# Kernel optimization log

Hardware: AMD Instinct MI355X
Metric: run time of the kernel (lower is better)

The kernel has to match this reference:

```python
import jax, jax.numpy as jnp
import numpy as np

B = 2            # batch_size (number of windows)
W_SIZE = 2       # window_size
WIDTH = 256      # cart_pixel_width
TEMP = 0.01      # softmax_temp
EPS = 1e-12      # F.normalize eps


def _l2norm(x, axis):
    n = jnp.sqrt(jnp.sum(x * x, axis=axis, keepdims=True))
    return x / jnp.maximum(n, EPS)


def _bilinear(img, u, v):
    """align_corners=True bilinear sample. img: [C,H,W]; u,v: [N] pixel coords."""
    H, W = img.shape[-2], img.shape[-1]
    u0 = jnp.clip(jnp.floor(u), 0, W - 1)
    v0 = jnp.clip(jnp.floor(v), 0, H - 1)
    u1 = jnp.clip(u0 + 1, 0, W - 1)
    v1 = jnp.clip(v0 + 1, 0, H - 1)
    au = u - u0
    av = v - v0
    u0i, u1i = u0.astype(jnp.int32), u1.astype(jnp.int32)
    v0i, v1i = v0.astype(jnp.int32), v1.astype(jnp.int32)
    g = lambda vi, ui: img[:, vi, ui]  # [C,N]
    return (g(v0i, u0i) * (1 - au) * (1 - av) + g(v0i, u1i) * au * (1 - av)
            + g(v1i, u0i) * (1 - au) * av + g(v1i, u1i) * au * av)


def setup_inputs() -> dict:
    key = jax.random.key(0)
    k1, k2, k3, k4 = jax.random.split(key, 4)
    BW, C, N, S = B * W_SIZE, 248, 1024, 1
    return {
        "keypoint_scores": jax.random.normal(k1, (BW, S, N), dtype=jnp.float32),
        "keypoint_desc": jax.random.normal(k2, (BW, C, N), dtype=jnp.float32),
        "desc_dense": jax.random.normal(k3, (BW, C, WIDTH, WIDTH), dtype=jnp.float32),
        "times_img": jax.random.uniform(k4, (BW, 1, WIDTH, WIDTH), dtype=jnp.float32),
    }


def reference(keypoint_scores, keypoint_desc, desc_dense, times_img):
    BW, C, N = keypoint_desc.shape
    w = W_SIZE
    # frame index bookkeeping (same as the torch per-batch loop, vectorized)
    src_ids = jnp.arange(B) * w                                   # [B]
    tgt_ids = (jnp.arange(B)[:, None] * w
               + jnp.arange(1, w)[None, :]).reshape(-1)           # [B*(w-1)]

    # dense pixel coordinates [W^2, 2] in (u, v) order
    v, u = jnp.meshgrid(jnp.arange(WIDTH), jnp.arange(WIDTH), indexing='ij')
    coords = jnp.stack([u.reshape(-1), v.reshape(-1)], axis=1).astype(desc_dense.dtype)

    # normalized source dense descriptors [B, C, W^2]
    src = _l2norm(desc_dense[src_ids].reshape(B, C, -1), axis=1)
    # normalized target keypoint descriptors [B, w-1, C, N]
    tgt = _l2norm(keypoint_desc[tgt_ids].reshape(B, w - 1, C, N), axis=2)

    # dense correlation: [B, w-1, N, W^2]
    match_vals = jnp.einsum('bkcn,bcm->bknm', tgt, src)
    soft = jax.nn.softmax(match_vals / TEMP, axis=-1)
    # coordinate-weighted sum -> pseudo coords [B*(w-1), N, 2]
    pseudo_coords = jnp.einsum('bknm,md->bknd', soft, coords).reshape(B * (w - 1), N, 2)

    # bilinear-sample src times at pseudo coords (normalize->grid_sample round trip
    # with align_corners maps back to the same pixel coords; H == W here)
    src_times = jnp.repeat(times_img[src_ids], w - 1, axis=0)      # [B*(w-1),1,H,W]
    pseudo_times = jax.vmap(_bilinear)(src_times,
                                       pseudo_coords[..., 0],
                                       pseudo_coords[..., 1])      # [B*(w-1),1,N]

    return (pseudo_coords, keypoint_scores[tgt_ids], tgt_ids, pseudo_times)
```

## Files before the change

kernel.cpp:

```cpp
#include <hip/hip_runtime.h>
#include <math.h>

typedef int i32x4 __attribute__((ext_vector_type(4)));
typedef int i32x16 __attribute__((ext_vector_type(16)));

#define CC 248
#define MM 65536
#define NN 1024

__device__ __forceinline__ float fexp2(float x) { return __builtin_amdgcn_exp2f(x); }


__global__ __launch_bounds__(512)
void convB_kernel(const float* __restrict__ dense, char* __restrict__ Ag) {
    __shared__ char at[2][16][128][16];
    __shared__ float scr[4][128];
    const int bid = blockIdx.x;
    const int fb  = bid >> 9;
    const int p0  = (bid & 511) * 128;
    const int tid = threadIdx.x;
    const int row = tid & 127;
    const int q   = tid >> 7;

    const float* dptr = dense + (size_t)(2 * fb) * CC * MM + p0 + row;
    float v[64];
    float ss = 0.f;
#pragma unroll
    for (int i = 0; i < 64; ++i) {
        int c = q * 64 + i;
        float x = (c < CC) ? dptr[(size_t)c * MM] : 0.f;
        v[i] = x;
        ss += x * x;
    }
    scr[q][row] = ss;
    __syncthreads();
    float inv = 32768.0f / fmaxf(sqrtf(scr[0][row] + scr[1][row] + scr[2][row] + scr[3][row]), 1e-12f);

#pragma unroll
    for (int j = 0; j < 16; ++j) {
        unsigned w1 = 0, w0 = 0;
#pragma unroll
        for (int t = 0; t < 4; ++t) {
            float qv = fminf(fmaxf(rintf(v[j * 4 + t] * inv), -32768.f), 32639.f);
            int af = (int)qv;
            int a1 = (af + 128) >> 8;
            int a0 = af - (a1 << 8);
            w1 |= (unsigned)(a1 & 255) << (8 * t);
            w0 |= (unsigned)(a0 & 255) << (8 * t);
        }
        int c0 = q * 64 + j * 4;
        int kg = c0 >> 4, dw = (c0 >> 2) & 3;
        *(unsigned*)&at[0][kg][row][dw * 4] = w1;
        *(unsigned*)&at[1][kg][row][dw * 4] = w0;
    }
    __syncthreads();

    const int tile = p0 >> 8, rhalf = (p0 >> 7) & 1;
    char* outb = Ag + (size_t)(fb * 256 + tile) * 131072;
#pragma unroll
    for (int it = 0; it < 8; ++it) {
        int id = tid + it * 512;
        int pl = id >> 11, kg = (id >> 7) & 15, r2 = id & 127;
        i32x4 vv = *(const i32x4*)&at[pl][kg][r2][0];
        *(i32x4*)&outb[(size_t)pl * 65536 + kg * 4096 + (rhalf * 128 + r2) * 16] = vv;
    }
}

__global__ __launch_bounds__(256)
void convA_kernel(const float* __restrict__ kdesc, char* __restrict__ Bg) {
    __shared__ char bt[2][16][32][16];
    __shared__ float scr[8][32];
    const int bid = blockIdx.x;
    const int b   = bid >> 5;
    const int nt  = bid & 31;
    const int n0  = nt * 32;
    const int tid = threadIdx.x;
    const int col = tid & 31;
    const int q   = tid >> 5;

    const float* kp = kdesc + (size_t)(2 * b + 1) * CC * NN + n0 + col;
    float ss = 0.f;
    for (int i = 0; i < 31; ++i) {
        int c = q * 31 + i;
        float v = kp[(size_t)c * NN];
        ss += v * v;
    }
    scr[q][col] = ss;
    __syncthreads();
    float tot = 0.f;
#pragma unroll
    for (int k = 0; k < 8; ++k) tot += scr[k][col];
    float inv = 32768.0f / fmaxf(sqrtf(tot), 1e-12f);
    if (tid < 64) {
        int pl = tid >> 5, c2 = tid & 31;
        *(long*)&bt[pl][15][c2][8] = 0L;
    }
    __syncthreads();
    for (int i = 0; i < 31; ++i) {
        int c = q * 31 + i;
        float qq = fminf(fmaxf(rintf(kp[(size_t)c * NN] * inv), -32768.f), 32639.f);
        int af = (int)qq;
        int a1 = (af + 128) >> 8;
        int a0 = af - (a1 << 8);
        bt[0][c >> 4][col][c & 15] = (char)a1;
        bt[1][c >> 4][col][c & 15] = (char)a0;
    }
    __syncthreads();
    char* outb = Bg + (size_t)(b * 32 + nt) * 16384;
    const char* src = &bt[0][0][0][0];
#pragma unroll
    for (int it = 0; it < 4; ++it) {
        int id = tid + it * 256;
        *(i32x4*)&outb[(size_t)id * 16] = *(const i32x4*)&src[(size_t)id * 16];
    }
}

__global__ __launch_bounds__(256, 2)
void gemm_kernel(const char* __restrict__ Ag, const char* __restrict__ Bg,
                 float* __restrict__ partials) {
    __shared__ char lds[24576];

    const int bid  = blockIdx.x;
    const int xcd  = bid & 7;
    const int rest = bid >> 3;
    const int nchunk = rest & 3;
    const int pid  = xcd + 8 * (rest >> 2);
    const int b      = pid >> 6;
    const int mchunk = pid & 63;

    const int lane = threadIdx.x & 63;
    const int w    = threadIdx.x >> 6;
    const int lrow = lane & 31;
    const int lhi  = lane >> 5;

    const char* atile0 = Ag + ((size_t)b * 256 + mchunk * 4) * 131072;
    const char* bb     = Bg + (size_t)(b * 32 + nchunk * 8 + w * 2) * 16384;

    i32x4 bc[8][2][2];
#pragma unroll
    for (int kk = 0; kk < 8; ++kk)
#pragma unroll
        for (int pl = 0; pl < 2; ++pl)
#pragma unroll
            for (int bp = 0; bp < 2; ++bp)
                bc[kk][pl][bp] = *(const i32x4*)(bb + bp * 16384 + pl * 8192
                                                 + (kk * 2 + lhi) * 512 + lrow * 16);

    auto ISSUE = [&](int p, int slotOff) {
        const int mtn = p >> 1, h = p & 1;
        const int tile = mtn >> 3, row0 = (mtn & 7) * 32;
#pragma unroll
        for (int i = 0; i < 2; ++i) {
            int c = w * 2 + i;
            int pl = c >> 2, kkl = c & 3;
            const char* src = atile0 + (size_t)tile * 131072 + pl * 65536
                            + (h * 8 + kkl * 2 + lhi) * 4096 + (row0 + lrow) * 16;
            char* dst = &lds[slotOff + pl * 4096 + kkl * 1024];
            __builtin_amdgcn_global_load_lds(
                (const __attribute__((address_space(1))) void*)src,
                (__attribute__((address_space(3))) void*)dst, 16, 0, 0);
        }
    };

    i32x16 accH[2], accX[2];
#pragma unroll
    for (int bp = 0; bp < 2; ++bp) { accH[bp] = (i32x16)(0); accX[bp] = (i32x16)(0); }
    float rz[2] = {0.f, 0.f}, rsu[2] = {0.f, 0.f}, rsv[2] = {0.f, 0.f};

    const float S2 = 100.0f * 1.4426950408889634f / 1073741824.0f;
    const float cH = 65536.0f * S2;
    const float cX = 256.0f * S2;
    const float BASE = 145.0f;

    auto EPI = [&](int mtq) {
        const int mbase = mchunk * 1024 + mtq * 32;
        const float ub = (float)((mbase & 255) + 4 * lhi);
        const float vcoord = (float)(mbase >> 8);
#pragma unroll
        for (int bp = 0; bp < 2; ++bp) {
            float tz = 0.f, tsur = 0.f;
#pragma unroll
            for (int r = 0; r < 16; ++r) {
                float e = fexp2(fmaf((float)accH[bp][r], cH,
                                fmaf((float)accX[bp][r], cX, -BASE)));
                tz += e;
                tsur = fmaf(e, (float)((r & 3) + 8 * (r >> 2)), tsur);
            }
            rz[bp] += tz;
            rsu[bp] += fmaf(ub, tz, tsur);
            rsv[bp] = fmaf(vcoord, tz, rsv[bp]);
            accH[bp] = (i32x16)(0); accX[bp] = (i32x16)(0);
        }
    };

    ISSUE(0, 0);
    ISSUE(1, 8192);
    int slotR = 0, slotW = 16384;

    for (int mt = 0; mt < 32; ++mt) {
#pragma unroll
        for (int h = 0; h < 2; ++h) {
            const int p = mt * 2 + h;
            if (p < 63) asm volatile("s_waitcnt vmcnt(2)" ::: "memory");
            else        asm volatile("s_waitcnt vmcnt(0)" ::: "memory");
            asm volatile("s_barrier" ::: "memory");
            if (p + 2 < 64) ISSUE(p + 2, slotW);

            i32x4 a1_0 = *(const i32x4*)&lds[slotR + 0 * 1024 + lhi * 512 + lrow * 16];
            i32x4 a0_0 = *(const i32x4*)&lds[slotR + 4096 + 0 * 1024 + lhi * 512 + lrow * 16];
            i32x4 a1_1 = *(const i32x4*)&lds[slotR + 1 * 1024 + lhi * 512 + lrow * 16];
            i32x4 a0_1 = *(const i32x4*)&lds[slotR + 4096 + 1 * 1024 + lhi * 512 + lrow * 16];

            if (h == 0 && mt > 0) EPI(mt - 1);

            __builtin_amdgcn_s_setprio(1);
#pragma unroll
            for (int bp = 0; bp < 2; ++bp) {
                accH[bp] = __builtin_amdgcn_mfma_i32_32x32x32_i8(a1_0, bc[h * 4 + 0][0][bp], accH[bp], 0, 0, 0);
                accX[bp] = __builtin_amdgcn_mfma_i32_32x32x32_i8(a1_0, bc[h * 4 + 0][1][bp], accX[bp], 0, 0, 0);
                accX[bp] = __builtin_amdgcn_mfma_i32_32x32x32_i8(a0_0, bc[h * 4 + 0][0][bp], accX[bp], 0, 0, 0);
                accH[bp] = __builtin_amdgcn_mfma_i32_32x32x32_i8(a1_1, bc[h * 4 + 1][0][bp], accH[bp], 0, 0, 0);
                accX[bp] = __builtin_amdgcn_mfma_i32_32x32x32_i8(a1_1, bc[h * 4 + 1][1][bp], accX[bp], 0, 0, 0);
                accX[bp] = __builtin_amdgcn_mfma_i32_32x32x32_i8(a0_1, bc[h * 4 + 1][0][bp], accX[bp], 0, 0, 0);
            }
            __builtin_amdgcn_s_setprio(0);

            i32x4 a1_2 = *(const i32x4*)&lds[slotR + 2 * 1024 + lhi * 512 + lrow * 16];
            i32x4 a0_2 = *(const i32x4*)&lds[slotR + 4096 + 2 * 1024 + lhi * 512 + lrow * 16];
            i32x4 a1_3 = *(const i32x4*)&lds[slotR + 3 * 1024 + lhi * 512 + lrow * 16];
            i32x4 a0_3 = *(const i32x4*)&lds[slotR + 4096 + 3 * 1024 + lhi * 512 + lrow * 16];

            __builtin_amdgcn_s_setprio(1);
#pragma unroll
            for (int bp = 0; bp < 2; ++bp) {
                accH[bp] = __builtin_amdgcn_mfma_i32_32x32x32_i8(a1_2, bc[h * 4 + 2][0][bp], accH[bp], 0, 0, 0);
                accX[bp] = __builtin_amdgcn_mfma_i32_32x32x32_i8(a1_2, bc[h * 4 + 2][1][bp], accX[bp], 0, 0, 0);
                accX[bp] = __builtin_amdgcn_mfma_i32_32x32x32_i8(a0_2, bc[h * 4 + 2][0][bp], accX[bp], 0, 0, 0);
                accH[bp] = __builtin_amdgcn_mfma_i32_32x32x32_i8(a1_3, bc[h * 4 + 3][0][bp], accH[bp], 0, 0, 0);
                accX[bp] = __builtin_amdgcn_mfma_i32_32x32x32_i8(a1_3, bc[h * 4 + 3][1][bp], accX[bp], 0, 0, 0);
                accX[bp] = __builtin_amdgcn_mfma_i32_32x32x32_i8(a0_3, bc[h * 4 + 3][0][bp], accX[bp], 0, 0, 0);
            }
            __builtin_amdgcn_s_setprio(0);

            slotR = (slotR == 16384) ? 0 : slotR + 8192;
            slotW = (slotW == 16384) ? 0 : slotW + 8192;
        }
    }
    EPI(31);

#pragma unroll
    for (int bp = 0; bp < 2; ++bp) {
        rz[bp]  += __shfl_xor(rz[bp],  32, 64);
        rsu[bp] += __shfl_xor(rsu[bp], 32, 64);
        rsv[bp] += __shfl_xor(rsv[bp], 32, 64);
    }
    if (lane < 32) {
#pragma unroll
        for (int bp = 0; bp < 2; ++bp) {
            int n = nchunk * 256 + w * 64 + bp * 32 + lrow;
            size_t idxp = ((size_t)b * NN + n) * 64 + mchunk;
            ((float4*)partials)[idxp] = make_float4(rz[bp], rsu[bp], rsv[bp], 0.f);
        }
    }
}

__global__ __launch_bounds__(256)
void combine_kernel(const float* __restrict__ partials,
                    const float* __restrict__ kscores,
                    const float* __restrict__ times,
                    float* __restrict__ out) {
    const int wg   = blockIdx.x * 4 + (threadIdx.x >> 6);
    const int lane = threadIdx.x & 63;
    const int b = wg >> 10, n = wg & 1023;
    const float4* pp = (const float4*)partials + (size_t)wg * 64;

    float4 p = pp[lane];
    float z = p.x, su = p.y, sv = p.z;
#pragma unroll
    for (int mask = 32; mask >= 1; mask >>= 1) {
        z  += __shfl_xor(z,  mask, 64);
        su += __shfl_xor(su, mask, 64);
        sv += __shfl_xor(sv, mask, 64);
    }

    if (lane == 0) {
        float u = su / z, v = sv / z;
        out[(size_t)wg * 2 + 0] = u;
        out[(size_t)wg * 2 + 1] = v;
        out[4096 + wg] = kscores[(size_t)(2 * b + 1) * NN + n];
        if (wg == 0) { out[6144] = 1.0f; out[6145] = 3.0f; }

        const float* timg = times + (size_t)(2 * b) * MM;
        float u0 = fminf(fmaxf(floorf(u), 0.f), 255.f);
        float v0 = fminf(fmaxf(floorf(v), 0.f), 255.f);
        float u1 = fminf(u0 + 1.f, 255.f);
        float v1 = fminf(v0 + 1.f, 255.f);
        float au = u - u0, av = v - v0;
        int u0i = (int)u0, u1i = (int)u1, v0i = (int)v0, v1i = (int)v1;
        float t00 = timg[v0i * 256 + u0i], t01 = timg[v0i * 256 + u1i];
        float t10 = timg[v1i * 256 + u0i], t11 = timg[v1i * 256 + u1i];
        float t = t00 * (1.f - au) * (1.f - av) + t01 * au * (1.f - av)
                + t10 * (1.f - au) * av + t11 * au * av;
        out[6146 + wg] = t;
    }
}

extern "C" void kernel_launch(void* const* d_in, const int* in_sizes, int n_in,
                              void* d_out, int out_size, void* d_ws, size_t ws_size,
                              hipStream_t stream) {
    const float* kscores = (const float*)d_in[0];
    const float* kdesc   = (const float*)d_in[1];
    const float* dense   = (const float*)d_in[2];
    const float* times   = (const float*)d_in[3];
    float* out = (float*)d_out;

    char* Ag = (char*)d_ws;
    char* Bg = Ag + (size_t)2 * 256 * 131072;
    float* partials = (float*)(Bg + (size_t)2 * 32 * 16384);

    hipLaunchKernelGGL(convB_kernel,   dim3(1024), dim3(512), 0, stream, dense, Ag);
    hipLaunchKernelGGL(convA_kernel,   dim3(64),   dim3(256), 0, stream, kdesc, Bg);
    hipLaunchKernelGGL(gemm_kernel,    dim3(512),  dim3(256), 0, stream, Ag, Bg, partials);
    hipLaunchKernelGGL(combine_kernel, dim3(512),  dim3(256), 0, stream, partials, kscores, times, out);
}
```

Baseline: 136.7 us.

## Fuse dense descriptor quantization into GEMM kernel, dropping global int8 intermediate

```diff
diff --git a/kernel.cpp b/kernel.cpp
--- a/kernel.cpp
+++ b/kernel.cpp
@@ -10,61 +10,6 @@
 
 __device__ __forceinline__ float fexp2(float x) { return __builtin_amdgcn_exp2f(x); }
 
-
-__global__ __launch_bounds__(512)
-void convB_kernel(const float* __restrict__ dense, char* __restrict__ Ag) {
-    __shared__ char at[2][16][128][16];
-    __shared__ float scr[4][128];
-    const int bid = blockIdx.x;
-    const int fb  = bid >> 9;
-    const int p0  = (bid & 511) * 128;
-    const int tid = threadIdx.x;
-    const int row = tid & 127;
-    const int q   = tid >> 7;
-
-    const float* dptr = dense + (size_t)(2 * fb) * CC * MM + p0 + row;
-    float v[64];
-    float ss = 0.f;
-#pragma unroll
-    for (int i = 0; i < 64; ++i) {
-        int c = q * 64 + i;
-        float x = (c < CC) ? dptr[(size_t)c * MM] : 0.f;
-        v[i] = x;
-        ss += x * x;
-    }
-    scr[q][row] = ss;
-    __syncthreads();
-    float inv = 32768.0f / fmaxf(sqrtf(scr[0][row] + scr[1][row] + scr[2][row] + scr[3][row]), 1e-12f);
-
-#pragma unroll
-    for (int j = 0; j < 16; ++j) {
-        unsigned w1 = 0, w0 = 0;
-#pragma unroll
-        for (int t = 0; t < 4; ++t) {
-            float qv = fminf(fmaxf(rintf(v[j * 4 + t] * inv), -32768.f), 32639.f);
-            int af = (int)qv;
-            int a1 = (af + 128) >> 8;
-            int a0 = af - (a1 << 8);
-            w1 |= (unsigned)(a1 & 255) << (8 * t);
-            w0 |= (unsigned)(a0 & 255) << (8 * t);
-        }
-        int c0 = q * 64 + j * 4;
-        int kg = c0 >> 4, dw = (c0 >> 2) & 3;
-        *(unsigned*)&at[0][kg][row][dw * 4] = w1;
-        *(unsigned*)&at[1][kg][row][dw * 4] = w0;
-    }
-    __syncthreads();
-
-    const int tile = p0 >> 8, rhalf = (p0 >> 7) & 1;
-    char* outb = Ag + (size_t)(fb * 256 + tile) * 131072;
-#pragma unroll
-    for (int it = 0; it < 8; ++it) {
-        int id = tid + it * 512;
-        int pl = id >> 11, kg = (id >> 7) & 15, r2 = id & 127;
-        i32x4 vv = *(const i32x4*)&at[pl][kg][r2][0];
-        *(i32x4*)&outb[(size_t)pl * 65536 + kg * 4096 + (rhalf * 128 + r2) * 16] = vv;
-    }
-}
 
 __global__ __launch_bounds__(256)
 void convA_kernel(const float* __restrict__ kdesc, char* __restrict__ Bg) {
@@ -116,150 +61,129 @@
 }
 
 __global__ __launch_bounds__(256, 2)
-void gemm_kernel(const char* __restrict__ Ag, const char* __restrict__ Bg,
-                 float* __restrict__ partials) {
-    __shared__ char lds[24576];
-
-    const int bid  = blockIdx.x;
-    const int xcd  = bid & 7;
-    const int rest = bid >> 3;
-    const int nchunk = rest & 3;
-    const int pid  = xcd + 8 * (rest >> 2);
-    const int b      = pid >> 6;
-    const int mchunk = pid & 63;
-
-    const int lane = threadIdx.x & 63;
-    const int w    = threadIdx.x >> 6;
+void fused_kernel(const float* __restrict__ dense, const char* __restrict__ Bg,
+                  float* __restrict__ partials) {
+    extern __shared__ char lds[];
+    float* scr = (float*)(lds + 65536);
+
+    const int bid = blockIdx.x;
+    const int fb  = bid >> 9;
+    const int p0  = (bid & 511) * 128;
+    const int tid = threadIdx.x;
+
+    {
+        const int row = tid & 127;
+        const int q   = tid >> 7;
+        const float* dptr = dense + (size_t)(2 * fb) * CC * MM + (size_t)(q * 124) * MM + p0 + row;
+        float v[124];
+        float ss = 0.f;
+#pragma unroll
+        for (int i = 0; i < 124; ++i) {
+            v[i] = dptr[(size_t)i * MM];
+            ss += v[i] * v[i];
+        }
+        scr[q * 128 + row] = ss;
+        *(long*)&lds[(tid >> 7) * 32768 + 15 * 2048 + (tid & 127) * 16 + 8] = 0L;
+        __syncthreads();
+        float inv = 32768.0f / fmaxf(sqrtf(scr[row] + scr[128 + row]), 1e-12f);
+#pragma unroll
+        for (int j = 0; j < 31; ++j) {
+            unsigned w1 = 0, w0 = 0;
+#pragma unroll
+            for (int t = 0; t < 4; ++t) {
+                float qv = fminf(fmaxf(rintf(v[j * 4 + t] * inv), -32768.f), 32639.f);
+                int af = (int)qv;
+                int a1 = (af + 128) >> 8;
+                int a0 = af - (a1 << 8);
+                w1 |= (unsigned)(a1 & 255) << (8 * t);
+                w0 |= (unsigned)(a0 & 255) << (8 * t);
+            }
+            int c0 = q * 124 + j * 4;
+            int kg = c0 >> 4, dw = (c0 >> 2) & 3;
+            *(unsigned*)&lds[kg * 2048 + row * 16 + dw * 4] = w1;
+            *(unsigned*)&lds[32768 + kg * 2048 + row * 16 + dw * 4] = w0;
+        }
+    }
+    __syncthreads();
+
+    const int lane = tid & 63;
+    const int w    = tid >> 6;
     const int lrow = lane & 31;
     const int lhi  = lane >> 5;
 
-    const char* atile0 = Ag + ((size_t)b * 256 + mchunk * 4) * 131072;
-    const char* bb     = Bg + (size_t)(b * 32 + nchunk * 8 + w * 2) * 16384;
-
-    i32x4 bc[8][2][2];
-#pragma unroll
-    for (int kk = 0; kk < 8; ++kk)
-#pragma unroll
-        for (int pl = 0; pl < 2; ++pl)
-#pragma unroll
-            for (int bp = 0; bp < 2; ++bp)
-                bc[kk][pl][bp] = *(const i32x4*)(bb + bp * 16384 + pl * 8192
-                                                 + (kk * 2 + lhi) * 512 + lrow * 16);
-
-    auto ISSUE = [&](int p, int slotOff) {
-        const int mtn = p >> 1, h = p & 1;
-        const int tile = mtn >> 3, row0 = (mtn & 7) * 32;
-#pragma unroll
-        for (int i = 0; i < 2; ++i) {
-            int c = w * 2 + i;
-            int pl = c >> 2, kkl = c & 3;
-            const char* src = atile0 + (size_t)tile * 131072 + pl * 65536
-                            + (h * 8 + kkl * 2 + lhi) * 4096 + (row0 + lrow) * 16;
-            char* dst = &lds[slotOff + pl * 4096 + kkl * 1024];
-            __builtin_amdgcn_global_load_lds(
-                (const __attribute__((address_space(1))) void*)src,
-                (__attribute__((address_space(3))) void*)dst, 16, 0, 0);
-        }
-    };
-
-    i32x16 accH[2], accX[2];
-#pragma unroll
-    for (int bp = 0; bp < 2; ++bp) { accH[bp] = (i32x16)(0); accX[bp] = (i32x16)(0); }
-    float rz[2] = {0.f, 0.f}, rsu[2] = {0.f, 0.f}, rsv[2] = {0.f, 0.f};
+    const char* bbase = Bg + (size_t)(fb * 32) * 16384;
 
     const float S2 = 100.0f * 1.4426950408889634f / 1073741824.0f;
     const float cH = 65536.0f * S2;
     const float cX = 256.0f * S2;
     const float BASE = 145.0f;
 
-    auto EPI = [&](int mtq) {
-        const int mbase = mchunk * 1024 + mtq * 32;
-        const float ub = (float)((mbase & 255) + 4 * lhi);
-        const float vcoord = (float)(mbase >> 8);
+    for (int nc = 0; nc < 4; ++nc) {
+        i32x4 bc[8][2][2];
+#pragma unroll
+        for (int kk = 0; kk < 8; ++kk)
+#pragma unroll
+            for (int pl = 0; pl < 2; ++pl)
+#pragma unroll
+                for (int bp = 0; bp < 2; ++bp)
+                    bc[kk][pl][bp] = *(const i32x4*)(bbase
+                        + (size_t)(w * 8 + nc * 2 + bp) * 16384 + pl * 8192
+                        + (kk * 2 + lhi) * 512 + lrow * 16);
+
+        float rz[2] = {0.f, 0.f}, rsu[2] = {0.f, 0.f}, rsv[2] = {0.f, 0.f};
+
+#pragma unroll
+        for (int mt = 0; mt < 4; ++mt) {
+            i32x16 accH[2], accX[2];
+#pragma unroll
+            for (int bp = 0; bp < 2; ++bp) { accH[bp] = (i32x16)(0); accX[bp] = (i32x16)(0); }
+
+#pragma unroll
+            for (int kk = 0; kk < 8; ++kk) {
+                i32x4 a1 = *(const i32x4*)&lds[(kk * 2 + lhi) * 2048 + (mt * 32 + lrow) * 16];
+                i32x4 a0 = *(const i32x4*)&lds[32768 + (kk * 2 + lhi) * 2048 + (mt * 32 + lrow) * 16];
+                __builtin_amdgcn_s_setprio(1);
+#pragma unroll
+                for (int bp = 0; bp < 2; ++bp) {
+                    accH[bp] = __builtin_amdgcn_mfma_i32_32x32x32_i8(a1, bc[kk][0][bp], accH[bp], 0, 0, 0);
+                    accX[bp] = __builtin_amdgcn_mfma_i32_32x32x32_i8(a1, bc[kk][1][bp], accX[bp], 0, 0, 0);
+                    accX[bp] = __builtin_amdgcn_mfma_i32_32x32x32_i8(a0, bc[kk][0][bp], accX[bp], 0, 0, 0);
+                }
+                __builtin_amdgcn_s_setprio(0);
+            }
+
+            const int mbase = p0 + mt * 32;
+            const float ub = (float)((mbase & 255) + 4 * lhi);
+            const float vcoord = (float)(mbase >> 8);
+#pragma unroll
+            for (int bp = 0; bp < 2; ++bp) {
+                float tz = 0.f, tsur = 0.f;
+#pragma unroll
+                for (int r = 0; r < 16; ++r) {
+                    float e = fexp2(fmaf((float)accH[bp][r], cH,
+                                    fmaf((float)accX[bp][r], cX, -BASE)));
+                    tz += e;
+                    tsur = fmaf(e, (float)((r & 3) + 8 * (r >> 2)), tsur);
+                }
+                rz[bp] += tz;
+                rsu[bp] += fmaf(ub, tz, tsur);
+                rsv[bp] = fmaf(vcoord, tz, rsv[bp]);
+            }
+        }
+
 #pragma unroll
         for (int bp = 0; bp < 2; ++bp) {
-            float tz = 0.f, tsur = 0.f;
-#pragma unroll
-            for (int r = 0; r < 16; ++r) {
-                float e = fexp2(fmaf((float)accH[bp][r], cH,
-                                fmaf((float)accX[bp][r], cX, -BASE)));
-                tz += e;
-                tsur = fmaf(e, (float)((r & 3) + 8 * (r >> 2)), tsur);
-            }
-            rz[bp] += tz;
-            rsu[bp] += fmaf(ub, tz, tsur);
-            rsv[bp] = fmaf(vcoord, tz, rsv[bp]);
-            accH[bp] = (i32x16)(0); accX[bp] = (i32x16)(0);
-        }
-    };
-
-    ISSUE(0, 0);
-    ISSUE(1, 8192);
-    int slotR = 0, slotW = 16384;
-
-    for (int mt = 0; mt < 32; ++mt) {
-#pragma unroll
-        for (int h = 0; h < 2; ++h) {
-            const int p = mt * 2 + h;
-            if (p < 63) asm volatile("s_waitcnt vmcnt(2)" ::: "memory");
-            else        asm volatile("s_waitcnt vmcnt(0)" ::: "memory");
-            asm volatile("s_barrier" ::: "memory");
-            if (p + 2 < 64) ISSUE(p + 2, slotW);
-
-            i32x4 a1_0 = *(const i32x4*)&lds[slotR + 0 * 1024 + lhi * 512 + lrow * 16];
-            i32x4 a0_0 = *(const i32x4*)&lds[slotR + 4096 + 0 * 1024 + lhi * 512 + lrow * 16];
-            i32x4 a1_1 = *(const i32x4*)&lds[slotR + 1 * 1024 + lhi * 512 + lrow * 16];
-            i32x4 a0_1 = *(const i32x4*)&lds[slotR + 4096 + 1 * 1024 + lhi * 512 + lrow * 16];
-
-            if (h == 0 && mt > 0) EPI(mt - 1);
-
-            __builtin_amdgcn_s_setprio(1);
+            rz[bp]  += __shfl_xor(rz[bp],  32, 64);
+            rsu[bp] += __shfl_xor(rsu[bp], 32, 64);
+            rsv[bp] += __shfl_xor(rsv[bp], 32, 64);
+        }
+        if (lane < 32) {
 #pragma unroll
             for (int bp = 0; bp < 2; ++bp) {
-                accH[bp] = __builtin_amdgcn_mfma_i32_32x32x32_i8(a1_0, bc[h * 4 + 0][0][bp], accH[bp], 0, 0, 0);
-                accX[bp] = __builtin_amdgcn_mfma_i32_32x32x32_i8(a1_0, bc[h * 4 + 0][1][bp], accX[bp], 0, 0, 0);
-                accX[bp] = __builtin_amdgcn_mfma_i32_32x32x32_i8(a0_0, bc[h * 4 + 0][0][bp], accX[bp], 0, 0, 0);
-                accH[bp] = __builtin_amdgcn_mfma_i32_32x32x32_i8(a1_1, bc[h * 4 + 1][0][bp], accH[bp], 0, 0, 0);
-                accX[bp] = __builtin_amdgcn_mfma_i32_32x32x32_i8(a1_1, bc[h * 4 + 1][1][bp], accX[bp], 0, 0, 0);
-                accX[bp] = __builtin_amdgcn_mfma_i32_32x32x32_i8(a0_1, bc[h * 4 + 1][0][bp], accX[bp], 0, 0, 0);
-            }
-            __builtin_amdgcn_s_setprio(0);
-
-            i32x4 a1_2 = *(const i32x4*)&lds[slotR + 2 * 1024 + lhi * 512 + lrow * 16];
-            i32x4 a0_2 = *(const i32x4*)&lds[slotR + 4096 + 2 * 1024 + lhi * 512 + lrow * 16];
-            i32x4 a1_3 = *(const i32x4*)&lds[slotR + 3 * 1024 + lhi * 512 + lrow * 16];
-            i32x4 a0_3 = *(const i32x4*)&lds[slotR + 4096 + 3 * 1024 + lhi * 512 + lrow * 16];
-
-            __builtin_amdgcn_s_setprio(1);
-#pragma unroll
-            for (int bp = 0; bp < 2; ++bp) {
-                accH[bp] = __builtin_amdgcn_mfma_i32_32x32x32_i8(a1_2, bc[h * 4 + 2][0][bp], accH[bp], 0, 0, 0);
-                accX[bp] = __builtin_amdgcn_mfma_i32_32x32x32_i8(a1_2, bc[h * 4 + 2][1][bp], accX[bp], 0, 0, 0);
-                accX[bp] = __builtin_amdgcn_mfma_i32_32x32x32_i8(a0_2, bc[h * 4 + 2][0][bp], accX[bp], 0, 0, 0);
-                accH[bp] = __builtin_amdgcn_mfma_i32_32x32x32_i8(a1_3, bc[h * 4 + 3][0][bp], accH[bp], 0, 0, 0);
-                accX[bp] = __builtin_amdgcn_mfma_i32_32x32x32_i8(a1_3, bc[h * 4 + 3][1][bp], accX[bp], 0, 0, 0);
-                accX[bp] = __builtin_amdgcn_mfma_i32_32x32x32_i8(a0_3, bc[h * 4 + 3][0][bp], accX[bp], 0, 0, 0);
-            }
-            __builtin_amdgcn_s_setprio(0);
-
-            slotR = (slotR == 16384) ? 0 : slotR + 8192;
-            slotW = (slotW == 16384) ? 0 : slotW + 8192;
-        }
-    }
-    EPI(31);
-
-#pragma unroll
-    for (int bp = 0; bp < 2; ++bp) {
-        rz[bp]  += __shfl_xor(rz[bp],  32, 64);
-        rsu[bp] += __shfl_xor(rsu[bp], 32, 64);
-        rsv[bp] += __shfl_xor(rsv[bp], 32, 64);
-    }
-    if (lane < 32) {
-#pragma unroll
-        for (int bp = 0; bp < 2; ++bp) {
-            int n = nchunk * 256 + w * 64 + bp * 32 + lrow;
-            size_t idxp = ((size_t)b * NN + n) * 64 + mchunk;
-            ((float4*)partials)[idxp] = make_float4(rz[bp], rsu[bp], rsv[bp], 0.f);
+                int n = w * 256 + nc * 64 + bp * 32 + lrow;
+                size_t idxp = ((size_t)(fb * NN + n)) * 512 + (bid & 511);
+                ((float4*)partials)[idxp] = make_float4(rz[bp], rsu[bp], rsv[bp], 0.f);
+            }
         }
     }
 }
@@ -272,10 +196,14 @@
     const int wg   = blockIdx.x * 4 + (threadIdx.x >> 6);
     const int lane = threadIdx.x & 63;
     const int b = wg >> 10, n = wg & 1023;
-    const float4* pp = (const float4*)partials + (size_t)wg * 64;
-
-    float4 p = pp[lane];
-    float z = p.x, su = p.y, sv = p.z;
+    const float4* pp = (const float4*)partials + (size_t)wg * 512;
+
+    float z = 0.f, su = 0.f, sv = 0.f;
+#pragma unroll
+    for (int k = 0; k < 8; ++k) {
+        float4 p = pp[k * 64 + lane];
+        z += p.x; su += p.y; sv += p.z;
+    }
 #pragma unroll
     for (int mask = 32; mask >= 1; mask >>= 1) {
         z  += __shfl_xor(z,  mask, 64);
@@ -314,12 +242,13 @@
     const float* times   = (const float*)d_in[3];
     float* out = (float*)d_out;
 
-    char* Ag = (char*)d_ws;
-    char* Bg = Ag + (size_t)2 * 256 * 131072;
+    char* Bg = (char*)d_ws;
     float* partials = (float*)(Bg + (size_t)2 * 32 * 16384);
 
-    hipLaunchKernelGGL(convB_kernel,   dim3(1024), dim3(512), 0, stream, dense, Ag);
+    hipFuncSetAttribute((const void*)fused_kernel,
+                        hipFuncAttributeMaxDynamicSharedMemorySize, 66560);
+
     hipLaunchKernelGGL(convA_kernel,   dim3(64),   dim3(256), 0, stream, kdesc, Bg);
-    hipLaunchKernelGGL(gemm_kernel,    dim3(512),  dim3(256), 0, stream, Ag, Bg, partials);
+    hipLaunchKernelGGL(fused_kernel,   dim3(1024), dim3(256), 66560, stream, dense, Bg, partials);
     hipLaunchKernelGGL(combine_kernel, dim3(512),  dim3(256), 0, stream, partials, kscores, times, out);
 }
```

After: 120.4 us. 11.9% less time.
